# Kernel tuning notes

Hardware: AMD Instinct MI355X
Metric: run time of the kernel (lower is better)

## Reference

```python
import jax, jax.numpy as jnp
import numpy as np

HID = 64
K = 24
CDIM = 8
B_GRAPHS = 32
NODES_PER_GRAPH = 1024
N = B_GRAPHS * NODES_PER_GRAPH


def _glorot(key, shape):
    fan_in, fan_out = shape[0], shape[1]
    lim = float(np.sqrt(6.0 / (fan_in + fan_out)))
    return jax.random.uniform(key, shape, jnp.float32, -lim, lim)


def setup_inputs() -> dict:
    key = jax.random.key(0)
    ks = jax.random.split(key, 16)
    inp = {
        "x_lc": jax.random.normal(ks[0], (N, 8), jnp.float32),
        # equal-sized graphs: batch id 0..31, 1024 nodes each, sorted
        "batch_lc": jnp.repeat(jnp.arange(B_GRAPHS, dtype=jnp.int64), NODES_PER_GRAPH),
        # lc_encode: Linear(8,64), Linear(64,64)
        "W1": _glorot(ks[1], (8, HID)), "b1": jnp.zeros((HID,), jnp.float32),
        "W2": _glorot(ks[2], (HID, HID)), "b2": jnp.zeros((HID,), jnp.float32),
        # 3 EdgeConv MLPs: Linear(2*64, 64) + ELU
        "Wc1": _glorot(ks[3], (2 * HID, HID)), "bc1": jnp.zeros((HID,), jnp.float32),
        "Wc2": _glorot(ks[4], (2 * HID, HID)), "bc2": jnp.zeros((HID,), jnp.float32),
        "Wc3": _glorot(ks[5], (2 * HID, HID)), "bc3": jnp.zeros((HID,), jnp.float32),
        # output head: 64->64->32->8 (dropout = identity in eval)
        "Wo1": _glorot(ks[6], (HID, 64)), "bo1": jnp.zeros((64,), jnp.float32),
        "Wo2": _glorot(ks[7], (64, 32)), "bo2": jnp.zeros((32,), jnp.float32),
        "Wo3": _glorot(ks[8], (32, CDIM)), "bo3": jnp.zeros((CDIM,), jnp.float32),
    }
    return inp


def _dynamic_edge_conv(x_bnd, W, b, k):
    """x_bnd: [B, n, d]. Rebuild kNN per graph on current features, then
    message = elu(cat[x_i, x_j - x_i] @ W + b), max-aggregate over neighbors."""
    def per_graph(x):  # x: [n, d]
        sq = jnp.sum(x * x, axis=-1)                       # [n]
        dist = sq[:, None] + sq[None, :] - 2.0 * (x @ x.T)  # [n, n]
        _, idx = jax.lax.top_k(-dist, k)                   # [n, k] (self included)
        xj = x[idx]                                        # [n, k, d]
        xi = x[:, None, :]                                 # [n, 1, d]
        e = jnp.concatenate([jnp.broadcast_to(xi, xj.shape), xj - xi], axis=-1)
        h = jax.nn.elu(e @ W + b)                          # [n, k, d_out]
        return jnp.max(h, axis=1)                          # [n, d_out]
    return jax.vmap(per_graph)(x_bnd)


def reference(x_lc, batch_lc, W1, b1, W2, b2, Wc1, bc1, Wc2, bc2, Wc3, bc3,
              Wo1, bo1, Wo2, bo2, Wo3, bo3):
    # lc_encode
    h = jax.nn.elu(x_lc @ W1 + b1)
    h = jax.nn.elu(h @ W2 + b2)                            # [N, HID]
    # equal-size graphs, sorted batch ids -> reshape to [B, n, d]
    num_graphs = int(batch_lc[-1]) + 1
    hb = h.reshape(num_graphs, -1, HID)
    f1 = _dynamic_edge_conv(hb, Wc1, bc1, K) + hb
    f2 = _dynamic_edge_conv(f1, Wc2, bc2, K) + f1
    f3 = _dynamic_edge_conv(f2, Wc3, bc3, K) + f2
    f3 = f3.reshape(-1, HID)
    # output head (dropout in eval mode = identity)
    o = jax.nn.elu(f3 @ Wo1 + bo1)
    o = jax.nn.elu(o @ Wo2 + bo2)
    out = o @ Wo3 + bo3                                    # [N, CDIM]
    return out, batch_lc
```

## Files before the change

### kernel.cpp

```cpp
#include <hip/hip_runtime.h>
#include <hip/hip_bf16.h>
#include <math.h>

#define NN   32768
#define BG   32
#define NPG  1024
#define HD   64
#define KK   24

#define FLTMAX 3.402823466e38f

typedef __attribute__((ext_vector_type(8))) short short8;
typedef __attribute__((ext_vector_type(4))) float f32x4;

__device__ __forceinline__ float elu1(float x) { return x > 0.f ? x : expm1f(x); }

__device__ __forceinline__ unsigned short f2bf(float x) {
  unsigned u = __float_as_uint(x);
  unsigned r = (u + 0x7FFFu + ((u >> 16) & 1u)) >> 16;
  return (unsigned short)r;
}
__device__ __forceinline__ float bf2f(unsigned short h) {
  return __uint_as_float(((unsigned)h) << 16);
}
__device__ __forceinline__ unsigned ordf(float f) {
  unsigned b = __float_as_uint(f);
  return (b & 0x80000000u) ? ~b : (b | 0x80000000u);
}

__device__ __forceinline__ void gl_lds16(const void* g, void* lds) {
  __builtin_amdgcn_global_load_lds(
      (const __attribute__((address_space(1))) unsigned int*)g,
      (__attribute__((address_space(3))) unsigned int*)lds, 16, 0, 0);
}

__global__ void __launch_bounds__(256) k_mlp_in(
    const float* __restrict__ x, const float* __restrict__ W1, const float* __restrict__ b1,
    const float* __restrict__ W2, const float* __restrict__ b2, float* __restrict__ F,
    const float* __restrict__ Wc0, const float* __restrict__ Wc1,
    const float* __restrict__ Wc2, unsigned char* __restrict__ Wf) {
  __shared__ float sW1[8*64];
  __shared__ float sW2[64*64];
  __shared__ float sb1[64];
  __shared__ float sb2[64];
  int t = threadIdx.x;
  if (blockIdx.x >= NN/128) {
    int lb = blockIdx.x - NN/128;
    const float* Wc = lb == 0 ? Wc0 : (lb == 1 ? Wc1 : Wc2);
    unsigned char* dst = Wf + (size_t)lb*32768;
    int f = t >> 1, colHalf = t & 1;
    int part = f & 1, nt = (f >> 1) & 7, oct = (f >> 4) & 3, ks = f >> 6;
#pragma unroll
    for (int cc = 0; cc < 8; ++cc) {
      int c8 = colHalf*8 + cc;
      int dp = nt*16 + c8;
      const float* wsrc = (dp < 64) ? (Wc + dp) : (Wc + 64*64 + (dp - 64));
      unsigned short sh[8];
#pragma unroll
      for (int j = 0; j < 8; ++j) {
        float w = wsrc[(ks*32 + oct*8 + j)*64];
        unsigned short hi = f2bf(w);
        sh[j] = part ? f2bf(w - bf2f(hi)) : hi;
      }
      *reinterpret_cast<int4*>(dst + f*256 + c8*16) = make_int4(
          (unsigned)sh[0] | ((unsigned)sh[1] << 16), (unsigned)sh[2] | ((unsigned)sh[3] << 16),
          (unsigned)sh[4] | ((unsigned)sh[5] << 16), (unsigned)sh[6] | ((unsigned)sh[7] << 16));
    }
    return;
  }
  for (int i = t; i < 8*64; i += 256) sW1[i] = W1[i];
  for (int i = t; i < 64*64; i += 256) sW2[i] = W2[i];
  if (t < 64) { sb1[t] = b1[t]; sb2[t] = b2[t]; }
  __syncthreads();
  int node = blockIdx.x*128 + (t & 127);
  int half = t >> 7;
  float xr[8];
#pragma unroll
  for (int i = 0; i < 8; ++i) xr[i] = x[node*8 + i];
  float h1[64];
#pragma unroll 8
  for (int k = 0; k < 64; ++k) {
    float a = sb1[k];
#pragma unroll
    for (int i = 0; i < 8; ++i) a += xr[i]*sW1[i*64+k];
    h1[k] = elu1(a);
  }
#pragma unroll 2
  for (int dd = 0; dd < 32; ++dd) {
    int d = half*32 + dd;
    float a = sb2[d];
#pragma unroll
    for (int k = 0; k < 64; ++k) a += h1[k]*sW2[k*64+d];
    F[node*64 + d] = elu1(a);
  }
}

__device__ __forceinline__ int conv_off(int node, int g) {
  return node*256 + ((((g & 7) ^ (node & 7)) | (g & 8)) << 4);
}

__global__ void __launch_bounds__(256) k_uv(
    const float* __restrict__ X, const unsigned char* __restrict__ Wf,
    const float* __restrict__ bc,
    float* __restrict__ U, float* __restrict__ V, float* __restrict__ SQ,
    unsigned char* __restrict__ XB) {
  __shared__ __align__(16) unsigned char sConv[64*256];
  __shared__ __align__(16) unsigned char sWf[128*256];
  __shared__ float sbc[64];
  int t = threadIdx.x;
  const int lane = t & 63, wave = t >> 6;
  const int g4 = lane >> 4, a15 = lane & 15;
  int b = blockIdx.x;
  int graph = (b & 7) + 8*(b >> 7);
  int nig0 = ((b >> 3) & 15) * 64;
  int base = graph*1024 + nig0;

  if (t < 64) sbc[t] = bc[t];

#pragma unroll
  for (int i = 0; i < 8; ++i) {
    int I = wave*8 + i;
    gl_lds16(Wf + (size_t)I*1024 + lane*16, (void*)(sWf + I*1024));
  }

  {
    int ln = t >> 2, q2 = t & 3;
    int ks = q2 >> 1, oh = (q2 & 1) * 2;
    const float* src = X + (size_t)(base + ln)*64 + ks*32 + oh*8;
    unsigned hu[8], lu[8];
    float sq = 0.f;
#pragma unroll
    for (int q = 0; q < 4; ++q) {
      float4 f = *reinterpret_cast<const float4*>(src + q*4);
      sq += f.x*f.x + f.y*f.y + f.z*f.z + f.w*f.w;
      unsigned short h0 = f2bf(f.x), h1 = f2bf(f.y), h2 = f2bf(f.z), h3 = f2bf(f.w);
      unsigned short l0 = f2bf(f.x - bf2f(h0)), l1 = f2bf(f.y - bf2f(h1));
      unsigned short l2 = f2bf(f.z - bf2f(h2)), l3 = f2bf(f.w - bf2f(h3));
      hu[q*2]   = (unsigned)h0 | ((unsigned)h1 << 16);
      hu[q*2+1] = (unsigned)h2 | ((unsigned)h3 << 16);
      lu[q*2]   = (unsigned)l0 | ((unsigned)l1 << 16);
      lu[q*2+1] = (unsigned)l2 | ((unsigned)l3 << 16);
    }
    sq += __shfl_xor(sq, 1);
    sq += __shfl_xor(sq, 2);
    if (q2 == 0) SQ[base + ln] = sq;
    unsigned char* gdst = XB + (((size_t)graph*2 + ks)*1024 + nig0 + ln)*128 + oh*16;
#pragma unroll
    for (int o = 0; o < 2; ++o) {
      int4 hp = make_int4(hu[o*4], hu[o*4+1], hu[o*4+2], hu[o*4+3]);
      int4 lp = make_int4(lu[o*4], lu[o*4+1], lu[o*4+2], lu[o*4+3]);
      *reinterpret_cast<int4*>(sConv + conv_off(ln, ks*8 + oh + o))     = hp;
      *reinterpret_cast<int4*>(sConv + conv_off(ln, ks*8 + 4 + oh + o)) = lp;
      *reinterpret_cast<int4*>(gdst + o*16)      = hp;
      *reinterpret_cast<int4*>(gdst + 64 + o*16) = lp;
    }
  }
  __syncthreads();

  f32x4 acc[8];
#pragma unroll
  for (int n = 0; n < 8; ++n) acc[n] = f32x4{0.f, 0.f, 0.f, 0.f};
#pragma unroll
  for (int ks = 0; ks < 2; ++ks) {
    int node = wave*16 + a15;
    short8 ah = *reinterpret_cast<const short8*>(sConv + conv_off(node, ks*8 + g4));
    short8 al = *reinterpret_cast<const short8*>(sConv + conv_off(node, ks*8 + 4 + g4));
#pragma unroll
    for (int nt = 0; nt < 8; ++nt) {
      int fb = ((ks*4 + g4)*8 + nt)*2;
      short8 bh = *reinterpret_cast<const short8*>(sWf + fb*256 + a15*16);
      short8 bl = *reinterpret_cast<const short8*>(sWf + (fb+1)*256 + a15*16);
      acc[nt] = __builtin_amdgcn_mfma_f32_16x16x32_bf16(ah, bh, acc[nt], 0, 0, 0);
      acc[nt] = __builtin_amdgcn_mfma_f32_16x16x32_bf16(ah, bl, acc[nt], 0, 0, 0);
      acc[nt] = __builtin_amdgcn_mfma_f32_16x16x32_bf16(al, bh, acc[nt], 0, 0, 0);
      acc[nt] = __builtin_amdgcn_mfma_f32_16x16x32_bf16(al, bl, acc[nt], 0, 0, 0);
    }
  }

#pragma unroll
  for (int nt = 0; nt < 4; ++nt) {
    float bcv = sbc[nt*16 + a15];
#pragma unroll
    for (int i = 0; i < 4; ++i) {
      size_t row = base + wave*16 + g4*4 + i;
      float p = acc[nt][i], q = acc[nt+4][i];
      U[row*64 + nt*16 + a15] = p - q + bcv;
      V[row*64 + nt*16 + a15] = q;
    }
  }
}

__device__ __forceinline__ int col_byte(int node, int granule) {
  return node*128 + ((granule ^ (node & 7)) << 4);
}

template<int LAST>
__global__ void __launch_bounds__(1024) k_knn(
    const unsigned char* __restrict__ XB, const float* __restrict__ SQ,
    const float* __restrict__ U, const float* __restrict__ V,
    float* __restrict__ F,
    const float* __restrict__ Wo1, const float* __restrict__ bo1,
    const float* __restrict__ Wo2, const float* __restrict__ bo2,
    const float* __restrict__ Wo3, const float* __restrict__ bo3,
    const int* __restrict__ batch, float* __restrict__ out, int out_size) {
  __shared__ __align__(16) unsigned char sBuf[49152];
  __shared__ __align__(16) unsigned char sRowB[64*272];
  __shared__ float sCsq[1024];
  __shared__ int nIdx[64*KK];

  int b = blockIdx.x;
  int g = (b & 7) + 8*(b >> 7);
  int rowBase = ((b >> 3) & 15) * 64;
  int gbase = g * NPG;
  int t = threadIdx.x;
  const int lane = t & 63, w = t >> 6;
  const int g4 = lane >> 4, a15 = lane & 15;
  const int rg = w >> 2, wc = w & 3;

  {
    int row = t >> 4, part = t & 15;
    int ks = part >> 3, o = part & 7;
    const unsigned char* src =
        XB + (((size_t)g*2 + ks)*1024 + rowBase + row)*128 + o*16;
    *reinterpret_cast<int4*>(sRowB + row*272 + part*16) =
        *reinterpret_cast<const int4*>(src);
    if (t < 256) {
      float4 q = *reinterpret_cast<const float4*>(SQ + gbase + t*4);
      *reinterpret_cast<float4*>(sCsq + t*4) = q;
    }
  }
  {
    int n = t >> 3, gq = t & 7;
    int srcChunk = (n << 3) + (gq ^ (n & 7));
    const unsigned char* sl0 = XB + (((size_t)g*2 + 0)*1024)*128;
    gl_lds16(sl0 + (size_t)srcChunk*16, (void*)(sBuf + 0*16384 + w*1024));
    const unsigned char* sl1 = XB + (((size_t)g*2 + 1)*1024)*128;
    gl_lds16(sl1 + (size_t)srcChunk*16, (void*)(sBuf + 1*16384 + w*1024));
  }
  __syncthreads();

  short8 ahf[2], alf[2];
#pragma unroll
  for (int ks = 0; ks < 2; ++ks) {
    ahf[ks] = *reinterpret_cast<const short8*>(
        sRowB + (rg*16 + a15)*272 + ks*128 + (g4 << 4));
    alf[ks] = *reinterpret_cast<const short8*>(
        sRowB + (rg*16 + a15)*272 + ks*128 + 64 + (g4 << 4));
  }

  f32x4 acc[16];
#pragma unroll
  for (int i = 0; i < 16; ++i) acc[i] = f32x4{0.f, 0.f, 0.f, 0.f};

#pragma unroll
  for (int c = 0; c < 16; ++c) {
    if (c) {
      if (c < 15) asm volatile("s_waitcnt vmcnt(1)" ::: "memory");
      else        asm volatile("s_waitcnt vmcnt(0)" ::: "memory");
      __builtin_amdgcn_sched_barrier(0);
      __builtin_amdgcn_s_barrier();
    }
    if (c < 14) {
      int cn = c + 2;
      const unsigned char* sl =
          XB + (((size_t)g*2 + (cn & 1))*1024 + (cn >> 1)*128)*128;
      int n = t >> 3, gq = t & 7;
      int srcChunk = (n << 3) + (gq ^ (n & 7));
      gl_lds16(sl + (size_t)srcChunk*16, (void*)(sBuf + (cn % 3)*16384 + w*1024));
    }
    const unsigned char* bufc = sBuf + (c % 3)*16384;
    short8 ah = ahf[c & 1], al = alf[c & 1];
#pragma unroll
    for (int tt = 0; tt < 2; ++tt) {
      int node = wc*32 + tt*16 + a15;
      short8 bh = *reinterpret_cast<const short8*>(bufc + col_byte(node, g4));
      short8 bl = *reinterpret_cast<const short8*>(bufc + col_byte(node, 4 + g4));
      int ai = (c >> 1)*2 + tt;
      acc[ai] = __builtin_amdgcn_mfma_f32_16x16x32_bf16(ah, bh, acc[ai], 0, 0, 0);
      acc[ai] = __builtin_amdgcn_mfma_f32_16x16x32_bf16(ah, bl, acc[ai], 0, 0, 0);
      acc[ai] = __builtin_amdgcn_mfma_f32_16x16x32_bf16(al, bh, acc[ai], 0, 0, 0);
      acc[ai] = __builtin_amdgcn_mfma_f32_16x16x32_bf16(al, bl, acc[ai], 0, 0, 0);
    }
  }

  float v[4][16];
  float* dL = (float*)sBuf;
#pragma unroll
  for (int e = 0; e < 8; ++e) {
    __syncthreads();
#pragma unroll
    for (int k2 = 0; k2 < 2; ++k2) {
      int ai = e*2 + k2;
      int lc = wc*32 + k2*16 + a15;
      float cs = sCsq[e*128 + lc];
#pragma unroll
      for (int i = 0; i < 4; ++i) {
        int r64 = rg*16 + g4*4 + i;
        dL[r64*128 + (lc ^ (((r64 >> 2) & 3) << 3))] = cs - 2.0f*acc[ai][i];
      }
    }
    __syncthreads();
#pragma unroll
    for (int m2 = 0; m2 < 2; ++m2)
#pragma unroll
      for (int r = 0; r < 4; ++r) {
        int rr = w*4 + r;
        v[r][e*2 + m2] = dL[rr*128 + ((m2*64 + lane) ^ (((rr >> 2) & 3) << 3))];
      }
  }
  __syncthreads();

  unsigned long long* sCmp = (unsigned long long*)sBuf;
  const unsigned long long mlt = (1ull << lane) - 1ull;

  unsigned uu[4];
#pragma unroll
  for (int r = 0; r < 4; ++r) {
    float bm = v[r][0];
#pragma unroll
    for (int m = 1; m < 16; ++m) bm = fminf(bm, v[r][m]);
    uu[r] = ordf(bm);
  }

  unsigned pp[4] = {0u, 0u, 0u, 0u};
#pragma unroll
  for (int bb = 31; bb >= 0; --bb) {
#pragma unroll
    for (int r = 0; r < 4; ++r) {
      unsigned q = pp[r] | (1u << bb);
      if ((int)__popcll(__ballot(uu[r] < q)) < KK) pp[r] = q;
    }
  }

  int total[4];
#pragma unroll
  for (int r = 0; r < 4; ++r) {
    int base = 0;
#pragma unroll
    for (int m = 0; m < 16; ++m) {
      unsigned ov = ordf(v[r][m]);
      bool f = ov <= pp[r];
      unsigned long long bal = __ballot(f);
      int slot = base + (int)__popcll(bal & mlt);
      if (f && slot < 64)
        sCmp[(w*4 + r)*64 + slot] =
            ((unsigned long long)ov << 32) | (unsigned)(lane + (m << 6));
      base += (int)__popcll(bal);
    }
    total[r] = base;
  }

  unsigned cu2[4]; int col2[4];
#pragma unroll
  for (int r = 0; r < 4; ++r) {
    unsigned long long kp = (lane < total[r]) ? sCmp[(w*4 + r)*64 + lane] : ~0ull;
    cu2[r] = (unsigned)(kp >> 32);
    col2[r] = (int)(unsigned)(kp & 0xFFFFFFFFull);
  }
  unsigned p2[4] = {0u, 0u, 0u, 0u};
#pragma unroll
  for (int bb = 31; bb >= 0; --bb) {
#pragma unroll
    for (int r = 0; r < 4; ++r) {
      unsigned q = p2[r] | (1u << bb);
      if ((int)__popcll(__ballot(cu2[r] < q)) < KK) p2[r] = q;
    }
  }
  int need[4]; bool tie[4];
#pragma unroll
  for (int r = 0; r < 4; ++r) {
    need[r] = KK - (int)__popcll(__ballot(cu2[r] < p2[r]));
    tie[r] = (cu2[r] == p2[r]);
  }
  unsigned p3[4] = {0u, 0u, 0u, 0u};
#pragma unroll
  for (int bb = 9; bb >= 0; --bb) {
#pragma unroll
    for (int r = 0; r < 4; ++r) {
      unsigned q = p3[r] | (1u << bb);
      if ((int)__popcll(__ballot(tie[r] && ((unsigned)col2[r] < q))) < need[r]) p3[r] = q;
    }
  }

  bool allfast = total[0] <= 64 && total[1] <= 64 && total[2] <= 64 && total[3] <= 64;
  if (allfast) {
#pragma unroll
    for (int r = 0; r < 4; ++r) {
      bool in24 = (cu2[r] < p2[r]) || (tie[r] && ((unsigned)col2[r] <= p3[r]));
      unsigned long long ball = __ballot(in24);
      int pos = (int)__popcll(ball & mlt);
      if (in24) nIdx[(w*4 + r)*KK + pos] = col2[r];
    }
  } else {
#pragma unroll
    for (int r = 0; r < 4; ++r) {
      unsigned selm = 0;
      for (int it = 0; it < KK; ++it) {
        float bv = FLTMAX; int bj = 0x7fffffff;
#pragma unroll
        for (int m = 0; m < 16; ++m) {
          float vv = ((selm >> m) & 1) ? FLTMAX : v[r][m];
          int col = lane + (m << 6);
          bool bsel = vv < bv; bv = bsel ? vv : bv; bj = bsel ? col : bj;
        }
#pragma unroll
        for (int s = 32; s; s >>= 1) {
          float ov = __shfl_xor(bv, s); int oj = __shfl_xor(bj, s);
          bool bsel = (ov < bv) || (ov == bv && oj < bj);
          bv = bsel ? ov : bv; bj = bsel ? oj : bj;
        }
        if (lane == (bj & 63)) selm |= 1u << (bj >> 6);
        if (lane == 0) nIdx[(w*4 + r)*KK + it] = bj;
      }
    }
  }

  if (!LAST) {
#pragma unroll
    for (int r = 0; r < 4; ++r) {
      int row = rowBase + w*4 + r;
      float mx = -FLTMAX;
#pragma unroll
      for (int tt = 0; tt < KK; ++tt) {
        int j = nIdx[(w*4 + r)*KK + tt];
        mx = fmaxf(mx, V[((size_t)(gbase + j))*64 + lane]);
      }
      size_t off = (size_t)(gbase + row)*64 + lane;
      F[off] += elu1(U[off] + mx);
    }
  } else {
    float* sOutF = (float*)sRowB;
#pragma unroll
    for (int r = 0; r < 4; ++r) {
      int row = rowBase + w*4 + r;
      float mx = -FLTMAX;
#pragma unroll
      for (int tt = 0; tt < KK; ++tt) {
        int j = nIdx[(w*4 + r)*KK + tt];
        mx = fmaxf(mx, V[((size_t)(gbase + j))*64 + lane]);
      }
      size_t off = (size_t)(gbase + row)*64 + lane;
      sOutF[(w*4 + r)*68 + lane] = F[off] + elu1(U[off] + mx);
    }
    __syncthreads();

    float* sW1o = (float*)sBuf;
    float* sW2o = sW1o + 64*64;
    float* sW3o = sW2o + 64*32;
    float* sB1o = sW3o + 32*8;
    float* sB2o = sB1o + 64;
    float* sB3o = sB2o + 32;
    float* sO1  = sB3o + 8;
    for (int i = t; i < 64*64; i += 1024) sW1o[i] = Wo1[i];
    for (int i = t; i < 64*32; i += 1024) sW2o[i] = Wo2[i];
    if (t < 256) sW3o[t] = Wo3[t];
    if (t < 64) sB1o[t] = bo1[t];
    if (t < 32) sB2o[t] = bo2[t];
    if (t < 8)  sB3o[t] = bo3[t];
    __syncthreads();

    int ln = t >> 3, qd = t & 7;
    if (t < 512) {
      float a1[8];
#pragma unroll
      for (int dd = 0; dd < 8; ++dd) a1[dd] = sB1o[qd*8 + dd];
#pragma unroll 4
      for (int k = 0; k < 64; ++k) {
        float fk = sOutF[ln*68 + k];
#pragma unroll
        for (int dd = 0; dd < 8; ++dd) a1[dd] += fk*sW1o[k*64 + qd*8 + dd];
      }
#pragma unroll
      for (int dd = 0; dd < 8; ++dd) sO1[ln*65 + qd*8 + dd] = elu1(a1[dd]);
    }
    __syncthreads();

    float* sO2 = (float*)sRowB;
    if (t < 512) {
      float a2[4];
#pragma unroll
      for (int dd = 0; dd < 4; ++dd) a2[dd] = sB2o[qd*4 + dd];
#pragma unroll 4
      for (int k = 0; k < 64; ++k) {
        float ok = sO1[ln*65 + k];
#pragma unroll
        for (int dd = 0; dd < 4; ++dd) a2[dd] += ok*sW2o[k*32 + qd*4 + dd];
      }
#pragma unroll
      for (int dd = 0; dd < 4; ++dd) sO2[ln*34 + qd*4 + dd] = elu1(a2[dd]);
    }
    __syncthreads();

    if (t < 512) {
      int nodeG = gbase + rowBase + ln;
      float a3 = sB3o[qd];
#pragma unroll
      for (int k = 0; k < 32; ++k) a3 += sO2[ln*34 + k]*sW3o[k*8 + qd];
      out[(size_t)nodeG*8 + qd] = a3;
      if (qd == 0 && out_size >= NN*9) out[(size_t)NN*8 + nodeG] = (float)batch[nodeG];
    }
  }
}

extern "C" void kernel_launch(void* const* d_in, const int* in_sizes, int n_in,
                              void* d_out, int out_size, void* d_ws, size_t ws_size,
                              hipStream_t stream) {
  const float* x     = (const float*)d_in[0];
  const int*   batch = (const int*)d_in[1];
  const float* W1 = (const float*)d_in[2];
  const float* b1 = (const float*)d_in[3];
  const float* W2 = (const float*)d_in[4];
  const float* b2 = (const float*)d_in[5];
  const float* Wc[3] = {(const float*)d_in[6], (const float*)d_in[8], (const float*)d_in[10]};
  const float* bc[3] = {(const float*)d_in[7], (const float*)d_in[9], (const float*)d_in[11]};
  const float* Wo1 = (const float*)d_in[12];
  const float* bo1 = (const float*)d_in[13];
  const float* Wo2 = (const float*)d_in[14];
  const float* bo2 = (const float*)d_in[15];
  const float* Wo3 = (const float*)d_in[16];
  const float* bo3 = (const float*)d_in[17];

  float* ws = (float*)d_ws;
  float* F0 = ws;
  float* U  = ws + (size_t)NN*64;
  float* V  = ws + (size_t)2*NN*64;
  float* SQ = ws + (size_t)3*NN*64;
  unsigned char* XB = (unsigned char*)(SQ + NN);
  unsigned char* WfG = XB + (size_t)NN*256;

  float* outF = (float*)d_out;
  k_mlp_in<<<NN/128 + 3, 256, 0, stream>>>(x, W1, b1, W2, b2, F0,
                                           Wc[0], Wc[1], Wc[2], WfG);
  for (int l = 0; l < 3; ++l) {
    k_uv <<<NN/64, 256, 0, stream>>>(F0, WfG + (size_t)l*32768, bc[l], U, V, SQ, XB);
    if (l < 2)
      k_knn<0><<<BG*(NPG/64), 1024, 0, stream>>>(XB, SQ, U, V, F0,
          Wo1, bo1, Wo2, bo2, Wo3, bo3, batch, outF, out_size);
    else
      k_knn<1><<<BG*(NPG/64), 1024, 0, stream>>>(XB, SQ, U, V, F0,
          Wo1, bo1, Wo2, bo2, Wo3, bo3, batch, outF, out_size);
  }
}
```

Measured before the change: 252.1 us.

## Fuse next layer's U/V projection into kNN kernel with ping-pong buffers

The kNN/aggregation kernel gains a mode that, after updating the node features, converts its 64-row tile to split bf16 hi/lo, writes squared norms and packed features for the next layer, and computes the next layer's U/V projection with MFMA inside the same block. The next layer's weights are prefetched into LDS during the radix-select phase, and U/V/SQ/XB are double-buffered so a block does not overwrite data other blocks are still reading. This removes two separate k_uv launches and their re-read of F. It adds LDS, register pressure and a launch_bounds occupancy hint, and falls back to the old path when the workspace is too small.

```diff
diff --git a/kernel.cpp b/kernel.cpp
--- a/kernel.cpp
+++ b/kernel.cpp
@@ -194,15 +194,18 @@
   return node*128 + ((granule ^ (node & 7)) << 4);
 }
 
-template<int LAST>
-__global__ void __launch_bounds__(1024) k_knn(
+template<int MODE>
+__global__ void __launch_bounds__(1024, 8) k_knn(
     const unsigned char* __restrict__ XB, const float* __restrict__ SQ,
     const float* __restrict__ U, const float* __restrict__ V,
     float* __restrict__ F,
     const float* __restrict__ Wo1, const float* __restrict__ bo1,
     const float* __restrict__ Wo2, const float* __restrict__ bo2,
     const float* __restrict__ Wo3, const float* __restrict__ bo3,
-    const int* __restrict__ batch, float* __restrict__ out, int out_size) {
+    const int* __restrict__ batch, float* __restrict__ out, int out_size,
+    const unsigned char* __restrict__ WfN, const float* __restrict__ bcN,
+    float* __restrict__ Un, float* __restrict__ Vn, float* __restrict__ SQn,
+    unsigned char* __restrict__ XBn) {
   __shared__ __align__(16) unsigned char sBuf[49152];
   __shared__ __align__(16) unsigned char sRowB[64*272];
   __shared__ float sCsq[1024];
@@ -357,6 +360,16 @@
     cu2[r] = (unsigned)(kp >> 32);
     col2[r] = (int)(unsigned)(kp & 0xFFFFFFFFull);
   }
+
+  if (MODE == 2) {
+    __syncthreads();
+#pragma unroll
+    for (int i = 0; i < 2; ++i) {
+      int I = w*2 + i;
+      gl_lds16(WfN + (size_t)I*1024 + lane*16, (void*)(sBuf + I*1024));
+    }
+  }
+
   unsigned p2[4] = {0u, 0u, 0u, 0u};
 #pragma unroll
   for (int bb = 31; bb >= 0; --bb) {
@@ -415,7 +428,7 @@
     }
   }
 
-  if (!LAST) {
+  if (MODE == 0) {
 #pragma unroll
     for (int r = 0; r < 4; ++r) {
       int row = rowBase + w*4 + r;
@@ -428,7 +441,7 @@
       size_t off = (size_t)(gbase + row)*64 + lane;
       F[off] += elu1(U[off] + mx);
     }
-  } else {
+  } else if (MODE == 1) {
     float* sOutF = (float*)sRowB;
 #pragma unroll
     for (int r = 0; r < 4; ++r) {
@@ -498,6 +511,90 @@
       for (int k = 0; k < 32; ++k) a3 += sO2[ln*34 + k]*sW3o[k*8 + qd];
       out[(size_t)nodeG*8 + qd] = a3;
       if (qd == 0 && out_size >= NN*9) out[(size_t)NN*8 + nodeG] = (float)batch[nodeG];
+    }
+  } else {
+    float* sOutF = (float*)sRowB;
+#pragma unroll
+    for (int r = 0; r < 4; ++r) {
+      int row = rowBase + w*4 + r;
+      float mx = -FLTMAX;
+#pragma unroll
+      for (int tt = 0; tt < KK; ++tt) {
+        int j = nIdx[(w*4 + r)*KK + tt];
+        mx = fmaxf(mx, V[((size_t)(gbase + j))*64 + lane]);
+      }
+      size_t off = (size_t)(gbase + row)*64 + lane;
+      float nf = F[off] + elu1(U[off] + mx);
+      F[off] = nf;
+      sOutF[(w*4 + r)*68 + lane] = nf;
+    }
+    asm volatile("s_waitcnt vmcnt(0)" ::: "memory");
+    __builtin_amdgcn_sched_barrier(0);
+    __syncthreads();
+
+    unsigned char* sConvT = sBuf + 32768;
+    if (t < 256) {
+      int ln = t >> 2, q2 = t & 3;
+      int ks = q2 >> 1, oh = (q2 & 1) * 2;
+      const float* src = sOutF + ln*68 + ks*32 + oh*8;
+      unsigned hu[8], lu[8];
+      float sq = 0.f;
+#pragma unroll
+      for (int q = 0; q < 4; ++q) {
+        float4 f = *reinterpret_cast<const float4*>(src + q*4);
+        sq += f.x*f.x + f.y*f.y + f.z*f.z + f.w*f.w;
+        unsigned short h0 = f2bf(f.x), h1 = f2bf(f.y), h2 = f2bf(f.z), h3 = f2bf(f.w);
+        unsigned short l0 = f2bf(f.x - bf2f(h0)), l1 = f2bf(f.y - bf2f(h1));
+        unsigned short l2 = f2bf(f.z - bf2f(h2)), l3 = f2bf(f.w - bf2f(h3));
+        hu[q*2]   = (unsigned)h0 | ((unsigned)h1 << 16);
+        hu[q*2+1] = (unsigned)h2 | ((unsigned)h3 << 16);
+        lu[q*2]   = (unsigned)l0 | ((unsigned)l1 << 16);
+        lu[q*2+1] = (unsigned)l2 | ((unsigned)l3 << 16);
+      }
+      sq += __shfl_xor(sq, 1);
+      sq += __shfl_xor(sq, 2);
+      if (q2 == 0) SQn[gbase + rowBase + ln] = sq;
+      unsigned char* gdst = XBn + (((size_t)g*2 + ks)*1024 + rowBase + ln)*128 + oh*16;
+#pragma unroll
+      for (int o = 0; o < 2; ++o) {
+        int4 hp = make_int4(hu[o*4], hu[o*4+1], hu[o*4+2], hu[o*4+3]);
+        int4 lp = make_int4(lu[o*4], lu[o*4+1], lu[o*4+2], lu[o*4+3]);
+        *reinterpret_cast<int4*>(sConvT + conv_off(ln, ks*8 + oh + o))     = hp;
+        *reinterpret_cast<int4*>(sConvT + conv_off(ln, ks*8 + 4 + oh + o)) = lp;
+        *reinterpret_cast<int4*>(gdst + o*16)      = hp;
+        *reinterpret_cast<int4*>(gdst + 64 + o*16) = lp;
+      }
+    }
+    __syncthreads();
+
+    f32x4 acc2[2];
+    acc2[0] = f32x4{0.f, 0.f, 0.f, 0.f};
+    acc2[1] = f32x4{0.f, 0.f, 0.f, 0.f};
+    int nodeT = (w & 3)*16 + a15;
+    int ntp = w >> 2;
+#pragma unroll
+    for (int ks2 = 0; ks2 < 2; ++ks2) {
+      short8 ah2 = *reinterpret_cast<const short8*>(sConvT + conv_off(nodeT, ks2*8 + g4));
+      short8 al2 = *reinterpret_cast<const short8*>(sConvT + conv_off(nodeT, ks2*8 + 4 + g4));
+#pragma unroll
+      for (int q = 0; q < 2; ++q) {
+        int nt = ntp + q*4;
+        int fb = ((ks2*4 + g4)*8 + nt)*2;
+        short8 bh = *reinterpret_cast<const short8*>(sBuf + fb*256 + a15*16);
+        short8 bl = *reinterpret_cast<const short8*>(sBuf + (fb+1)*256 + a15*16);
+        acc2[q] = __builtin_amdgcn_mfma_f32_16x16x32_bf16(ah2, bh, acc2[q], 0, 0, 0);
+        acc2[q] = __builtin_amdgcn_mfma_f32_16x16x32_bf16(ah2, bl, acc2[q], 0, 0, 0);
+        acc2[q] = __builtin_amdgcn_mfma_f32_16x16x32_bf16(al2, bh, acc2[q], 0, 0, 0);
+        acc2[q] = __builtin_amdgcn_mfma_f32_16x16x32_bf16(al2, bl, acc2[q], 0, 0, 0);
+      }
+    }
+    float bcv = bcN[ntp*16 + a15];
+#pragma unroll
+    for (int i = 0; i < 4; ++i) {
+      size_t row = (size_t)gbase + rowBase + (w & 3)*16 + g4*4 + i;
+      float p = acc2[0][i], q = acc2[1][i];
+      Un[row*64 + ntp*16 + a15] = p - q + bcv;
+      Vn[row*64 + ntp*16 + a15] = q;
     }
   }
 }
@@ -520,24 +617,58 @@
   const float* Wo3 = (const float*)d_in[16];
   const float* bo3 = (const float*)d_in[17];
 
-  float* ws = (float*)d_ws;
-  float* F0 = ws;
-  float* U  = ws + (size_t)NN*64;
-  float* V  = ws + (size_t)2*NN*64;
-  float* SQ = ws + (size_t)3*NN*64;
-  unsigned char* XB = (unsigned char*)(SQ + NN);
-  unsigned char* WfG = XB + (size_t)NN*256;
-
   float* outF = (float*)d_out;
-  k_mlp_in<<<NN/128 + 3, 256, 0, stream>>>(x, W1, b1, W2, b2, F0,
-                                           Wc[0], Wc[1], Wc[2], WfG);
-  for (int l = 0; l < 3; ++l) {
-    k_uv <<<NN/64, 256, 0, stream>>>(F0, WfG + (size_t)l*32768, bc[l], U, V, SQ, XB);
-    if (l < 2)
-      k_knn<0><<<BG*(NPG/64), 1024, 0, stream>>>(XB, SQ, U, V, F0,
-          Wo1, bo1, Wo2, bo2, Wo3, bo3, batch, outF, out_size);
-    else
-      k_knn<1><<<BG*(NPG/64), 1024, 0, stream>>>(XB, SQ, U, V, F0,
-          Wo1, bo1, Wo2, bo2, Wo3, bo3, batch, outF, out_size);
-  }
-}
+  const size_t NEED = (size_t)(5*NN*64 + 2*NN)*4 + (size_t)2*NN*256 + 98304;
+
+  if (ws_size >= NEED) {
+    float* ws = (float*)d_ws;
+    float* F0  = ws;
+    float* U0  = F0 + (size_t)NN*64;
+    float* V0  = U0 + (size_t)NN*64;
+    float* U1  = V0 + (size_t)NN*64;
+    float* V1  = U1 + (size_t)NN*64;
+    float* SQ0 = V1 + (size_t)NN*64;
+    float* SQ1 = SQ0 + NN;
+    unsigned char* XB0 = (unsigned char*)(SQ1 + NN);
+    unsigned char* XB1 = XB0 + (size_t)NN*256;
+    unsigned char* WfG = XB1 + (size_t)NN*256;
+
+    k_mlp_in<<<NN/128 + 3, 256, 0, stream>>>(x, W1, b1, W2, b2, F0,
+                                             Wc[0], Wc[1], Wc[2], WfG);
+    k_uv<<<NN/64, 256, 0, stream>>>(F0, WfG, bc[0], U0, V0, SQ0, XB0);
+    k_knn<2><<<BG*(NPG/64), 1024, 0, stream>>>(XB0, SQ0, U0, V0, F0,
+        Wo1, bo1, Wo2, bo2, Wo3, bo3, batch, outF, out_size,
+        WfG + 32768, bc[1], U1, V1, SQ1, XB1);
+    k_knn<2><<<BG*(NPG/64), 1024, 0, stream>>>(XB1, SQ1, U1, V1, F0,
+        Wo1, bo1, Wo2, bo2, Wo3, bo3, batch, outF, out_size,
+        WfG + 65536, bc[2], U0, V0, SQ0, XB0);
+    k_knn<1><<<BG*(NPG/64), 1024, 0, stream>>>(XB0, SQ0, U0, V0, F0,
+        Wo1, bo1, Wo2, bo2, Wo3, bo3, batch, outF, out_size,
+        (const unsigned char*)0, (const float*)0,
+        (float*)0, (float*)0, (float*)0, (unsigned char*)0);
+  } else {
+    float* ws = (float*)d_ws;
+    float* F0 = ws;
+    float* U  = ws + (size_t)NN*64;
+    float* V  = ws + (size_t)2*NN*64;
+    float* SQ = ws + (size_t)3*NN*64;
+    unsigned char* XB = (unsigned char*)(SQ + NN);
+    unsigned char* WfG = XB + (size_t)NN*256;
+
+    k_mlp_in<<<NN/128 + 3, 256, 0, stream>>>(x, W1, b1, W2, b2, F0,
+                                             Wc[0], Wc[1], Wc[2], WfG);
+    for (int l = 0; l < 3; ++l) {
+      k_uv<<<NN/64, 256, 0, stream>>>(F0, WfG + (size_t)l*32768, bc[l], U, V, SQ, XB);
+      if (l < 2)
+        k_knn<0><<<BG*(NPG/64), 1024, 0, stream>>>(XB, SQ, U, V, F0,
+            Wo1, bo1, Wo2, bo2, Wo3, bo3, batch, outF, out_size,
+            (const unsigned char*)0, (const float*)0,
+            (float*)0, (float*)0, (float*)0, (unsigned char*)0);
+      else
+        k_knn<1><<<BG*(NPG/64), 1024, 0, stream>>>(XB, SQ, U, V, F0,
+            Wo1, bo1, Wo2, bo2, Wo3, bo3, batch, outF, out_size,
+            (const unsigned char*)0, (const float*)0,
+            (float*)0, (float*)0, (float*)0, (unsigned char*)0);
+    }
+  }
+}
```

Result: slower. 399.3 us (+58.4%).
